# Optimization experiments

Hardware: AMD Instinct MI355X
Metric: run time of the kernel (lower is better)

The kernel has to match this reference:

```python
import jax, jax.numpy as jnp
import numpy as np

LN_EPS = 1e-5


def _layer_norm(x, g, b):
    mu = x.mean(-1, keepdims=True)
    var = ((x - mu) ** 2).mean(-1, keepdims=True)
    return (x - mu) / jnp.sqrt(var + LN_EPS) * g + b


def _process_memory(mem, mem_W, mem_b, ln_g, ln_b):
    # deep memory MLP: Linear -> LayerNorm -> SiLU per layer (dropout = identity in eval)
    h = mem
    for i in range(mem_W.shape[0]):
        h = jax.nn.silu(_layer_norm(h @ mem_W[i] + mem_b[i], ln_g[i], ln_b[i]))
    return h


def setup_inputs() -> dict:
    key = jax.random.key(0)
    B, S, D, M, L = 32, 2048, 1024, 1024, 2
    ks = jax.random.split(key, 12)
    s = 0.02
    inp = {
        'inputs': jax.random.normal(ks[0], (B, S, D), dtype=jnp.float32),
        'memory_state': jnp.zeros((B, M), dtype=jnp.float32),
        'momentum_state': jnp.zeros((B, M), dtype=jnp.float32),
        # projections (stored [in, out], equivalent to torch Linear weight.T)
        'Wk': jax.random.normal(ks[1], (D, M)) * s, 'bk': jnp.zeros((M,)),
        'Wv': jax.random.normal(ks[2], (D, M)) * s, 'bv': jnp.zeros((M,)),
        # deep memory layers, stacked over num_layers
        'mem_W': jax.random.normal(ks[3], (L, M, M)) * s,
        'mem_b': jnp.zeros((L, M)),
        'ln_g': jnp.ones((L, M)),
        'ln_b': jnp.zeros((L, M)),
        # gates: in = D + M
        'Wf': jax.random.normal(ks[4], (D + M, M)) * s, 'bf': jnp.zeros((M,)),
        'Wm': jax.random.normal(ks[5], (D + M, M)) * s, 'bm': jnp.zeros((M,)),
        'Wu': jax.random.normal(ks[6], (D + M, M)) * s, 'bu': jnp.zeros((M,)),
        'eta': jnp.ones((1,)) * 0.9,
        'theta': jnp.ones((1,)) * 0.1,
    }
    return inp


def reference(inputs, memory_state, momentum_state, Wk, bk, Wv, bv,
              mem_W, mem_b, ln_g, ln_b, Wf, bf, Wm, bm, Wu, bu, eta, theta):
    keys = inputs @ Wk + bk      # [B,S,M]
    values = inputs @ Wv + bv    # [B,S,M]

    def assoc_loss(mem):
        mo = _process_memory(mem, mem_W, mem_b, ln_g, ln_b)      # [B,M]
        pred = jnp.einsum('bsm,bm->bs', keys, mo)                # bmm(keys, mo^T)
        diff = pred[..., None] - values                          # expand to [B,S,M]
        return 0.5 * jnp.mean(diff ** 2)

    surprise_grad = jax.grad(assoc_loss)(memory_state)           # [B,M]

    pooled = inputs.mean(axis=1)                                 # [B,D]
    gate_in = jnp.concatenate([pooled, memory_state], axis=-1)   # [B,D+M]
    forget_g = jax.nn.sigmoid(gate_in @ Wf + bf)
    update_g = jax.nn.sigmoid(gate_in @ Wu + bu)
    # momentum_gate computed in source but unused in the update
    _ = jax.nn.sigmoid(gate_in @ Wm + bm)

    new_momentum = eta * momentum_state + theta * surprise_grad
    new_memory = (1.0 - forget_g) * memory_state + update_g * new_momentum

    processed = _process_memory(new_memory, mem_W, mem_b, ln_g, ln_b)
    return processed, jax.lax.stop_gradient(new_memory)
```

## Files before the change

### kernel.cpp

```cpp
#include <hip/hip_runtime.h>
#include <math.h>

#define Bc 32
#define Sc 2048
#define Dc 1024
#define Mc 1024
#define LNEPS 1e-5f
#define SCv (1.f/67108864.f)

__device__ __forceinline__ float4 f4add(float4 a, float4 b) {
    return make_float4(a.x + b.x, a.y + b.y, a.z + b.z, a.w + b.w);
}

__device__ __forceinline__ void dreduce(float& a, float& b, float* sm) {
#pragma unroll
    for (int o = 32; o; o >>= 1) { a += __shfl_xor(a, o); b += __shfl_xor(b, o); }
    int w = threadIdx.x >> 6;
    if ((threadIdx.x & 63) == 0) { sm[w] = a; sm[4 + w] = b; }
    __syncthreads();
    a = sm[0] + sm[1] + sm[2] + sm[3];
    b = sm[4] + sm[5] + sm[6] + sm[7];
    __syncthreads();
}

__device__ __forceinline__ void wreduce(float& a, float& b) {
#pragma unroll
    for (int o = 32; o; o >>= 1) { a += __shfl_xor(a, o); b += __shfl_xor(b, o); }
}

__device__ __forceinline__ void load_A128(float* Atile, const float* A, int b0, int k0) {
    for (int i = threadIdx.x; i < 1024; i += 256) {
        int r = i >> 7, c = i & 127;
        Atile[i] = A[(size_t)(b0 + r) * 1024 + k0 + c];
    }
}

__device__ __forceinline__ void nt_inner128v(const float* Atile, const float* W, int k0, int n0,
                                             float* P, int ks, int b0) {
    int lane = threadIdx.x & 63, bl = threadIdx.x >> 6;
    int n4 = lane & 15, kg = lane >> 4;
    const float* a0 = Atile + bl * 128;
    const float* a1 = Atile + (bl + 4) * 128;
    const float4* Wp = (const float4*)(W + (size_t)k0 * 1024 + n0);
    float4 acc0 = make_float4(0.f, 0.f, 0.f, 0.f);
    float4 acc1 = make_float4(0.f, 0.f, 0.f, 0.f);
#pragma unroll 8
    for (int i = 0; i < 32; ++i) {
        int k = i * 4 + kg;
        float4 w4 = Wp[(size_t)k * 256 + n4];
        float av0 = a0[k], av1 = a1[k];
        acc0.x = fmaf(av0, w4.x, acc0.x); acc0.y = fmaf(av0, w4.y, acc0.y);
        acc0.z = fmaf(av0, w4.z, acc0.z); acc0.w = fmaf(av0, w4.w, acc0.w);
        acc1.x = fmaf(av1, w4.x, acc1.x); acc1.y = fmaf(av1, w4.y, acc1.y);
        acc1.z = fmaf(av1, w4.z, acc1.z); acc1.w = fmaf(av1, w4.w, acc1.w);
    }
#pragma unroll
    for (int o = 16; o <= 32; o <<= 1) {
        acc0.x += __shfl_xor(acc0.x, o); acc0.y += __shfl_xor(acc0.y, o);
        acc0.z += __shfl_xor(acc0.z, o); acc0.w += __shfl_xor(acc0.w, o);
        acc1.x += __shfl_xor(acc1.x, o); acc1.y += __shfl_xor(acc1.y, o);
        acc1.z += __shfl_xor(acc1.z, o); acc1.w += __shfl_xor(acc1.w, o);
    }
    if (kg == 0) {
        size_t base = (size_t)ks * 32768 + n0 + 4 * n4;
        *(float4*)&P[base + (size_t)(b0 + bl) * 1024] = acc0;
        *(float4*)&P[base + (size_t)(b0 + bl + 4) * 1024] = acc1;
    }
}

__device__ __forceinline__ void t_inner(const float* Asl, const float* W,
                                        int dbase, int m0, float* outp) {
    int lane = threadIdx.x & 63, wv = threadIdx.x >> 6;
    int half = lane >> 5, m4 = lane & 31;
    float4 a4 = ((const float4*)Asl)[m4];
    int d0 = dbase + wv * 64 + half;
    float res = 0.f;
#pragma unroll 8
    for (int p = 0; p < 32; ++p) {
        int d = d0 + p * 2;
        float4 w4 = ((const float4*)(W + (size_t)d * 1024 + m0))[m4];
        float v = w4.x * a4.x + w4.y * a4.y + w4.z * a4.z + w4.w * a4.w;
#pragma unroll
        for (int o = 1; o < 32; o <<= 1) v += __shfl_xor(v, o);
        res = (m4 == p) ? v : res;
    }
    outp[wv * 64 + m4 * 2 + half] = res;
}

__global__ __launch_bounds__(256) void k_front(const float* __restrict__ Wv, const float* __restrict__ bv,
                        const float* __restrict__ mem, const float* __restrict__ W0,
                        float* __restrict__ wv_row, float* __restrict__ bvsum,
                        float* __restrict__ P1a) {
    __shared__ float shm[1032];
    int bid = blockIdx.x, tid = threadIdx.x;
    if (bid < 256) {
        float s1 = 0.f, s2 = 0.f, s3 = 0.f, s4 = 0.f;
        for (int m = tid; m < 1024; m += 256) {
            s1 += Wv[(size_t)bid * 1024 + m];
            s2 += Wv[(size_t)(bid + 256) * 1024 + m];
            s3 += Wv[(size_t)(bid + 512) * 1024 + m];
            s4 += Wv[(size_t)(bid + 768) * 1024 + m];
        }
        dreduce(s1, s2, shm + 1024);
        dreduce(s3, s4, shm + 1024);
        if (tid == 0) {
            wv_row[bid] = s1; wv_row[bid + 256] = s2;
            wv_row[bid + 512] = s3; wv_row[bid + 768] = s4;
        }
        if (bid == 0) {
            float v = 0.f, d2 = 0.f;
            for (int m = tid; m < 1024; m += 256) v += bv[m];
            dreduce(v, d2, shm + 1024);
            if (tid == 0) *bvsum = v;
        }
    } else {
        int t = bid - 256;
        int n0 = (t & 15) * 64, b0 = ((t >> 4) & 3) * 8, ks = t >> 6, k0 = ks * 128;
        load_A128(shm, mem, b0, k0);
        __syncthreads();
        nt_inner128v(shm, W0, k0, n0, P1a, ks, b0);
    }
}

__global__ __launch_bounds__(256) void k_gemm_ln(const float* __restrict__ P, const float* __restrict__ bias,
                          const float* __restrict__ g, const float* __restrict__ be,
                          const float* __restrict__ W1, float* __restrict__ Pout) {
    __shared__ float shm[1040];
    int bid = blockIdx.x, tid = threadIdx.x;
    int n0 = (bid & 15) * 64, b0 = ((bid >> 4) & 3) * 8, ks = bid >> 6, k0 = ks * 128;
    float* Atile = shm; float* stats = shm + 1024;
    int wv = tid >> 6, lane = tid & 63;
    const float4* b4 = (const float4*)bias;
    for (int rr = 0; rr < 2; ++rr) {
        int r = wv + rr * 4, b = b0 + r;
        float s = 0.f, sq = 0.f;
#pragma unroll
        for (int q = 0; q < 4; ++q) {
            int m4 = lane + 64 * q;
            float4 z4 = b4[m4];
#pragma unroll
            for (int k2 = 0; k2 < 8; ++k2) {
                float4 v = ((const float4*)(P + (size_t)k2 * 32768 + (size_t)b * 1024))[m4];
                z4 = f4add(z4, v);
            }
            int c0 = 4 * m4 - k0;
            if ((unsigned)c0 < 128u) *(float4*)(Atile + r * 128 + c0) = z4;
            s += z4.x + z4.y + z4.z + z4.w;
            sq += z4.x * z4.x + z4.y * z4.y + z4.z * z4.z + z4.w * z4.w;
        }
        wreduce(s, sq);
        if (lane == 0) {
            float mean = s * (1.f / 1024.f);
            stats[r] = mean;
            stats[8 + r] = rsqrtf(sq * (1.f / 1024.f) - mean * mean + LNEPS);
        }
    }
    __syncthreads();
    for (int i = tid; i < 1024; i += 256) {
        int r = i >> 7, c = i & 127, m = k0 + c;
        float xh = (Atile[i] - stats[r]) * stats[8 + r];
        float y = fmaf(xh, g[m], be[m]);
        float sg = 1.f / (1.f + __expf(-y));
        Atile[i] = y * sg;
    }
    __syncthreads();
    nt_inner128v(Atile, W1, k0, n0, Pout, ks, b0);
}

__global__ __launch_bounds__(256) void k_wpart(const float* __restrict__ P2a, const float* __restrict__ memb1,
                        const float* __restrict__ lng1, const float* __restrict__ lnb1,
                        const float* __restrict__ bk, const float* __restrict__ Wk,
                        float* __restrict__ wpart, float* __restrict__ cbpart) {
    __shared__ float shm[136];
    int bid = blockIdx.x, tid = threadIdx.x;
    int dc = bid & 3, b = (bid >> 2) & 31, mc = bid >> 7, m0 = mc * 128;
    float* red = shm + 128;
    float4 z4 = ((const float4*)memb1)[tid];
#pragma unroll
    for (int k2 = 0; k2 < 8; ++k2) {
        float4 v = ((const float4*)(P2a + (size_t)k2 * 32768 + (size_t)b * 1024))[tid];
        z4 = f4add(z4, v);
    }
    float s = z4.x + z4.y + z4.z + z4.w;
    float sq = z4.x * z4.x + z4.y * z4.y + z4.z * z4.z + z4.w * z4.w;
    int c0 = 4 * tid - m0;
    if ((unsigned)c0 < 128u) *(float4*)(shm + c0) = z4;
    dreduce(s, sq, red);
    float mean = s * (1.f / 1024.f);
    float rstd = rsqrtf(sq * (1.f / 1024.f) - mean * mean + LNEPS);
    if (tid < 128) {
        int m = m0 + tid;
        float xh = (shm[tid] - mean) * rstd;
        float y = fmaf(xh, lng1[m], lnb1[m]);
        float sg = 1.f / (1.f + __expf(-y));
        shm[tid] = y * sg;
    }
    __syncthreads();
    if (dc == 0) {
        float c = (tid < 128) ? bk[m0 + tid] * shm[tid] : 0.f;
        float d2 = 0.f;
        dreduce(c, d2, red);
        if (tid == 0) cbpart[mc * 32 + b] = c;
    }
    t_inner(shm, Wk, dc * 256, m0, wpart + (size_t)(mc * 32 + b) * 1024 + dc * 256);
}

__global__ __launch_bounds__(256) void k_bigpass(const float* __restrict__ X, const float* __restrict__ wpart,
                          const float* __restrict__ wv_row, const float* __restrict__ cbpart,
                          const float* __restrict__ bvsum,
                          float* __restrict__ t_part, float* __restrict__ p_part,
                          float* __restrict__ rs_part) {
    __shared__ float red[4][1024];
    __shared__ float rsum_s[4];
    int b = blockIdx.y, ch = blockIdx.x;
    int wv = threadIdx.x >> 6, lane = threadIdx.x & 63;
    float4 wreg[4], tacc[4], pacc[4];
    const float4* wp4 = (const float4*)wpart;
    const float4* wr4 = (const float4*)wv_row;
#pragma unroll
    for (int j = 0; j < 4; ++j) {
        int d4 = lane + 64 * j;
        float4 a = make_float4(0.f, 0.f, 0.f, 0.f);
#pragma unroll
        for (int mc = 0; mc < 8; ++mc) a = f4add(a, wp4[(size_t)(mc * 32 + b) * 256 + d4]);
        float4 wr = wr4[d4];
        wreg[j].x = 1024.f * a.x - wr.x;
        wreg[j].y = 1024.f * a.y - wr.y;
        wreg[j].z = 1024.f * a.z - wr.z;
        wreg[j].w = 1024.f * a.w - wr.w;
        tacc[j] = make_float4(0.f, 0.f, 0.f, 0.f);
        pacc[j] = make_float4(0.f, 0.f, 0.f, 0.f);
    }
    float cbs = 0.f;
#pragma unroll
    for (int mc = 0; mc < 8; ++mc) cbs += cbpart[mc * 32 + b];
    float cbv = 1024.f * cbs - *bvsum;
    float rloc = 0.f;
    int s0r = ch * 64 + wv * 16;
#pragma unroll 2
    for (int i = 0; i < 16; ++i) {
        const float4* xr = (const float4*)(X + ((size_t)b * Sc + s0r + i) * Dc);
        float4 x[4]; float pp = 0.f;
#pragma unroll
        for (int j = 0; j < 4; ++j) {
            x[j] = xr[lane + 64 * j];
            pp += x[j].x * wreg[j].x + x[j].y * wreg[j].y + x[j].z * wreg[j].z + x[j].w * wreg[j].w;
        }
#pragma unroll
        for (int o = 32; o; o >>= 1) pp += __shfl_xor(pp, o);
        float r = pp + cbv;
        rloc += r;
#pragma unroll
        for (int j = 0; j < 4; ++j) {
            tacc[j].x = fmaf(x[j].x, r, tacc[j].x);
            tacc[j].y = fmaf(x[j].y, r, tacc[j].y);
            tacc[j].z = fmaf(x[j].z, r, tacc[j].z);
            tacc[j].w = fmaf(x[j].w, r, tacc[j].w);
            pacc[j].x += x[j].x; pacc[j].y += x[j].y;
            pacc[j].z += x[j].z; pacc[j].w += x[j].w;
        }
    }
    float4* redv = (float4*)red[wv];
#pragma unroll
    for (int j = 0; j < 4; ++j) redv[lane + 64 * j] = tacc[j];
    if (lane == 0) rsum_s[wv] = rloc;
    __syncthreads();
    size_t pb = ((size_t)b * 32 + ch) * 1024;
    for (int j = 0; j < 4; ++j) {
        int d = threadIdx.x + 256 * j;
        t_part[pb + d] = red[0][d] + red[1][d] + red[2][d] + red[3][d];
    }
    if (threadIdx.x == 0) rs_part[b * 32 + ch] = rsum_s[0] + rsum_s[1] + rsum_s[2] + rsum_s[3];
    __syncthreads();
#pragma unroll
    for (int j = 0; j < 4; ++j) redv[lane + 64 * j] = pacc[j];
    __syncthreads();
    for (int j = 0; j < 4; ++j) {
        int d = threadIdx.x + 256 * j;
        p_part[pb + d] = red[0][d] + red[1][d] + red[2][d] + red[3][d];
    }
}

__global__ __launch_bounds__(256) void k_gates(const float* __restrict__ t_part, const float* __restrict__ p_part,
                        const float* __restrict__ mem,
                        const float* __restrict__ Wk, const float* __restrict__ Wf,
                        const float* __restrict__ Wu,
                        float* __restrict__ Pg, float* __restrict__ Pfp, float* __restrict__ Pup,
                        float* __restrict__ Pfm, float* __restrict__ Pum) {
    __shared__ float Atile[1024];
    int bid = blockIdx.x, tid = threadIdx.x;
    int z = bid >> 9, t = bid & 511;
    int n0 = (t & 15) * 64, b0 = ((t >> 4) & 3) * 8, ks = t >> 6, k0 = ks * 128;
    if (z >= 3) {
        load_A128(Atile, mem, b0, k0);
        __syncthreads();
        if (z == 3) nt_inner128v(Atile, Wf + (size_t)1024 * 1024, k0, n0, Pfm, ks, b0);
        else        nt_inner128v(Atile, Wu + (size_t)1024 * 1024, k0, n0, Pum, ks, b0);
        return;
    }
    const float* src = (z == 0) ? t_part : p_part;
    float scale = (z == 0) ? 1.f : (1.f / 2048.f);
    {
        int r = tid >> 5, c4 = tid & 31;
        int b = b0 + r;
        const float4* base = (const float4*)(src + (size_t)b * 32 * 1024 + k0) + c4;
        float4 acc = make_float4(0.f, 0.f, 0.f, 0.f);
#pragma unroll 8
        for (int ch = 0; ch < 32; ++ch) acc = f4add(acc, base[(size_t)ch * 256]);
        acc.x *= scale; acc.y *= scale; acc.z *= scale; acc.w *= scale;
        *(float4*)(Atile + r * 128 + 4 * c4) = acc;
    }
    __syncthreads();
    if (z == 0)      nt_inner128v(Atile, Wk, k0, n0, Pg, ks, b0);
    else if (z == 1) nt_inner128v(Atile, Wf, k0, n0, Pfp, ks, b0);
    else             nt_inner128v(Atile, Wu, k0, n0, Pup, ks, b0);
}

__global__ __launch_bounds__(256) void k_lnbwd_gemmT(const float* __restrict__ Pz, const float* __restrict__ bias,
                              const float* __restrict__ g, const float* __restrict__ be,
                              const float* __restrict__ Pgrad, int mode,
                              const float* __restrict__ bk, const float* __restrict__ rs_part,
                              const float* __restrict__ W, float* __restrict__ Pout) {
    __shared__ float shm[392];
    int bid = blockIdx.x, tid = threadIdx.x;
    int dc = bid & 3, b = (bid >> 2) & 31, mc = bid >> 7, m0 = mc * 128;
    float* red = shm + 384;
    float rsb = 0.f;
    if (mode) {
        float v = (tid < 32) ? rs_part[b * 32 + tid] : 0.f, d2 = 0.f;
        dreduce(v, d2, red);
        rsb = v;
    }
    float4 z4 = ((const float4*)bias)[tid];
#pragma unroll
    for (int k2 = 0; k2 < 8; ++k2) {
        float4 v = ((const float4*)(Pz + (size_t)k2 * 32768 + (size_t)b * 1024))[tid];
        z4 = f4add(z4, v);
    }
    float s = z4.x + z4.y + z4.z + z4.w;
    float sq = z4.x * z4.x + z4.y * z4.y + z4.z * z4.z + z4.w * z4.w;
    dreduce(s, sq, red);
    float mean = s * (1.f / 1024.f);
    float rstd = rsqrtf(sq * (1.f / 1024.f) - mean * mean + LNEPS);
    float4 g4 = make_float4(0.f, 0.f, 0.f, 0.f);
#pragma unroll
    for (int k2 = 0; k2 < 8; ++k2) {
        float4 v = ((const float4*)(Pgrad + (size_t)k2 * 32768 + (size_t)b * 1024))[tid];
        g4 = f4add(g4, v);
    }
    if (mode) {
        float4 bk4 = ((const float4*)bk)[tid];
        g4.x = SCv * (g4.x + bk4.x * rsb);
        g4.y = SCv * (g4.y + bk4.y * rsb);
        g4.z = SCv * (g4.z + bk4.z * rsb);
        g4.w = SCv * (g4.w + bk4.w * rsb);
    }
    float4 gg = ((const float4*)g)[tid], bb = ((const float4*)be)[tid];
    float sa = 0.f, sax = 0.f;
    float4 a4, xh4;
    {
        xh4.x = (z4.x - mean) * rstd;
        float y = fmaf(xh4.x, gg.x, bb.x);
        float sg2 = 1.f / (1.f + __expf(-y));
        a4.x = g4.x * (sg2 * (1.f + y * (1.f - sg2))) * gg.x;
        sa += a4.x; sax += a4.x * xh4.x;
        xh4.y = (z4.y - mean) * rstd;
        y = fmaf(xh4.y, gg.y, bb.y);
        sg2 = 1.f / (1.f + __expf(-y));
        a4.y = g4.y * (sg2 * (1.f + y * (1.f - sg2))) * gg.y;
        sa += a4.y; sax += a4.y * xh4.y;
        xh4.z = (z4.z - mean) * rstd;
        y = fmaf(xh4.z, gg.z, bb.z);
        sg2 = 1.f / (1.f + __expf(-y));
        a4.z = g4.z * (sg2 * (1.f + y * (1.f - sg2))) * gg.z;
        sa += a4.z; sax += a4.z * xh4.z;
        xh4.w = (z4.w - mean) * rstd;
        y = fmaf(xh4.w, gg.w, bb.w);
        sg2 = 1.f / (1.f + __expf(-y));
        a4.w = g4.w * (sg2 * (1.f + y * (1.f - sg2))) * gg.w;
        sa += a4.w; sax += a4.w * xh4.w;
    }
    int c0 = 4 * tid - m0;
    if ((unsigned)c0 < 128u) {
        *(float4*)(shm + c0) = a4;
        *(float4*)(shm + 128 + c0) = xh4;
    }
    dreduce(sa, sax, red);
    float ma = sa * (1.f / 1024.f), mx = sax * (1.f / 1024.f);
    if (tid < 128) shm[256 + tid] = rstd * (shm[tid] - ma - shm[128 + tid] * mx);
    __syncthreads();
    t_inner(shm + 256, W, dc * 256, m0, Pout + (size_t)(mc * 32 + b) * 1024 + dc * 256);
}

__global__ __launch_bounds__(256) void k_upd_g3(const float* __restrict__ Pfm, const float* __restrict__ Pfp,
                         const float* __restrict__ Pum, const float* __restrict__ Pup,
                         const float* __restrict__ surp,
                         const float* __restrict__ bf, const float* __restrict__ bu,
                         const float* __restrict__ mem, const float* __restrict__ mom,
                         const float* __restrict__ eta, const float* __restrict__ theta,
                         const float* __restrict__ W0, float* __restrict__ P3a,
                         float* __restrict__ out_nm) {
    __shared__ float Atile[1024];
    int bid = blockIdx.x, tid = threadIdx.x;
    int n0idx = bid & 15, n0 = n0idx * 64, b0 = ((bid >> 4) & 3) * 8, ks = bid >> 6, k0 = ks * 128;
    float etav = eta[0], thv = theta[0];
    int r = tid >> 5, c4 = tid & 31, b = b0 + r;
    int m4 = (k0 >> 2) + c4;
    float4 zf = ((const float4*)bf)[m4];
    float4 zu = ((const float4*)bu)[m4];
    float4 sv = make_float4(0.f, 0.f, 0.f, 0.f);
#pragma unroll
    for (int k2 = 0; k2 < 8; ++k2) {
        size_t ob4 = (size_t)k2 * 8192 + (size_t)b * 256 + m4;
        zf = f4add(zf, f4add(((const float4*)Pfm)[ob4], ((const float4*)Pfp)[ob4]));
        zu = f4add(zu, f4add(((const float4*)Pum)[ob4], ((const float4*)Pup)[ob4]));
        sv = f4add(sv, ((const float4*)surp)[ob4]);
    }
    float4 me = ((const float4*)mem)[(size_t)b * 256 + m4];
    float4 mo = ((const float4*)mom)[(size_t)b * 256 + m4];
    float4 nm;
    {
        float f = 1.f / (1.f + __expf(-zf.x)), u = 1.f / (1.f + __expf(-zu.x));
        nm.x = (1.f - f) * me.x + u * (etav * mo.x + thv * sv.x);
        f = 1.f / (1.f + __expf(-zf.y)); u = 1.f / (1.f + __expf(-zu.y));
        nm.y = (1.f - f) * me.y + u * (etav * mo.y + thv * sv.y);
        f = 1.f / (1.f + __expf(-zf.z)); u = 1.f / (1.f + __expf(-zu.z));
        nm.z = (1.f - f) * me.z + u * (etav * mo.z + thv * sv.z);
        f = 1.f / (1.f + __expf(-zf.w)); u = 1.f / (1.f + __expf(-zu.w));
        nm.w = (1.f - f) * me.w + u * (etav * mo.w + thv * sv.w);
    }
    *(float4*)(Atile + r * 128 + 4 * c4) = nm;
    if (n0idx == 0) ((float4*)out_nm)[(size_t)b * 256 + m4] = nm;
    __syncthreads();
    nt_inner128v(Atile, W0, k0, n0, P3a, ks, b0);
}

__global__ __launch_bounds__(256) void k_final(const float* __restrict__ P4a, const float* __restrict__ memb1,
                        const float* __restrict__ lng1, const float* __restrict__ lnb1,
                        float* __restrict__ out) {
    __shared__ float sm[8];
    int b = blockIdx.x, tid = threadIdx.x;
    float4 z4 = ((const float4*)memb1)[tid];
#pragma unroll
    for (int k2 = 0; k2 < 8; ++k2) {
        float4 v = ((const float4*)(P4a + (size_t)k2 * 32768 + (size_t)b * 1024))[tid];
        z4 = f4add(z4, v);
    }
    float s = z4.x + z4.y + z4.z + z4.w;
    float sq = z4.x * z4.x + z4.y * z4.y + z4.z * z4.z + z4.w * z4.w;
    dreduce(s, sq, sm);
    float mean = s * (1.f / 1024.f);
    float rstd = rsqrtf(sq * (1.f / 1024.f) - mean * mean + LNEPS);
    float4 gg = ((const float4*)lng1)[tid], bb = ((const float4*)lnb1)[tid];
    float4 o;
    {
        float xh = (z4.x - mean) * rstd, y = fmaf(xh, gg.x, bb.x);
        o.x = y / (1.f + __expf(-y));
        xh = (z4.y - mean) * rstd; y = fmaf(xh, gg.y, bb.y);
        o.y = y / (1.f + __expf(-y));
        xh = (z4.z - mean) * rstd; y = fmaf(xh, gg.z, bb.z);
        o.z = y / (1.f + __expf(-y));
        xh = (z4.w - mean) * rstd; y = fmaf(xh, gg.w, bb.w);
        o.w = y / (1.f + __expf(-y));
    }
    ((float4*)out)[(size_t)b * 256 + tid] = o;
}

extern "C" void kernel_launch(void* const* d_in, const int* in_sizes, int n_in,
                              void* d_out, int out_size, void* d_ws, size_t ws_size,
                              hipStream_t stream) {
    const float* X    = (const float*)d_in[0];
    const float* mem  = (const float*)d_in[1];
    const float* mom  = (const float*)d_in[2];
    const float* Wk   = (const float*)d_in[3];
    const float* bk   = (const float*)d_in[4];
    const float* Wv   = (const float*)d_in[5];
    const float* bv   = (const float*)d_in[6];
    const float* memW = (const float*)d_in[7];
    const float* memb = (const float*)d_in[8];
    const float* lng  = (const float*)d_in[9];
    const float* lnb  = (const float*)d_in[10];
    const float* Wf   = (const float*)d_in[11];
    const float* bf   = (const float*)d_in[12];
    const float* Wu   = (const float*)d_in[15];
    const float* bu   = (const float*)d_in[16];
    const float* eta  = (const float*)d_in[17];
    const float* theta= (const float*)d_in[18];
    float* out = (float*)d_out;

    const size_t BM = (size_t)Bc * Mc;
    float* ws = (float*)d_ws;
    float* P1a    = ws;
    float* P2a    = ws + 8 * BM;
    float* wpart  = ws + 16 * BM;
    float* Pg     = ws + 24 * BM;
    float* Pfp    = ws + 32 * BM;
    float* Pup    = ws + 40 * BM;
    float* Pfm    = ws + 48 * BM;
    float* Pum    = ws + 56 * BM;
    float* ghp    = ws + 64 * BM;
    float* surp   = ws + 72 * BM;
    float* P3a    = ws + 80 * BM;
    float* P4a    = ws + 88 * BM;
    float* t_part = ws + 96 * BM;
    float* p_part = ws + 128 * BM;
    float* wv_row = ws + 160 * BM;
    float* bvsum  = wv_row + 1024;
    float* cbpart = bvsum + 1;
    float* rs_part= cbpart + 256;

    const float* W0 = memW;
    const float* W1 = memW + (size_t)Mc * Mc;

    k_front<<<768, 256, 0, stream>>>(Wv, bv, mem, W0, wv_row, bvsum, P1a);
    k_gemm_ln<<<512, 256, 0, stream>>>(P1a, memb, lng, lnb, W1, P2a);
    k_wpart<<<1024, 256, 0, stream>>>(P2a, memb + 1024, lng + 1024, lnb + 1024, bk, Wk, wpart, cbpart);
    k_bigpass<<<dim3(32, 32), 256, 0, stream>>>(X, wpart, wv_row, cbpart, bvsum, t_part, p_part, rs_part);
    k_gates<<<2560, 256, 0, stream>>>(t_part, p_part, mem, Wk, Wf, Wu, Pg, Pfp, Pup, Pfm, Pum);
    k_lnbwd_gemmT<<<1024, 256, 0, stream>>>(P2a, memb + 1024, lng + 1024, lnb + 1024, Pg, 1, bk, rs_part, W1, ghp);
    k_lnbwd_gemmT<<<1024, 256, 0, stream>>>(P1a, memb, lng, lnb, ghp, 0, bk, rs_part, W0, surp);
    k_upd_g3<<<512, 256, 0, stream>>>(Pfm, Pfp, Pum, Pup, surp, bf, bu, mem, mom, eta, theta, W0, P3a, out + BM);
    k_gemm_ln<<<512, 256, 0, stream>>>(P3a, memb, lng, lnb, W1, P4a);
    k_final<<<32, 256, 0, stream>>>(P4a, memb + 1024, lng + 1024, lnb + 1024, out);
}
```

Baseline: 165.3 us.

## Remap block indices for XCD locality and hoist chunk reductions into a separate kernel

```diff
diff --git a/kernel.cpp b/kernel.cpp
--- a/kernel.cpp
+++ b/kernel.cpp
@@ -26,6 +26,21 @@
 __device__ __forceinline__ void wreduce(float& a, float& b) {
 #pragma unroll
     for (int o = 32; o; o >>= 1) { a += __shfl_xor(a, o); b += __shfl_xor(b, o); }
+}
+
+__device__ __forceinline__ void nt_map(int t, int& n0i, int& b0i, int& ks) {
+    int xcd = t & 7, rest = t >> 3;
+    b0i = rest & 3;
+    int q = rest >> 2;
+    int s = q * 8 + xcd;
+    ks = s >> 4; n0i = s & 15;
+}
+__device__ __forceinline__ void t_map(int t, int& dc, int& b, int& mc) {
+    int xcd = t & 7, rest = t >> 3;
+    b = rest & 31;
+    int q = rest >> 5;
+    int s = q * 8 + xcd;
+    dc = s >> 3; mc = s & 7;
 }
 
 __device__ __forceinline__ void load_A128(float* Atile, const float* A, int b0, int k0) {
@@ -114,8 +129,9 @@
             if (tid == 0) *bvsum = v;
         }
     } else {
-        int t = bid - 256;
-        int n0 = (t & 15) * 64, b0 = ((t >> 4) & 3) * 8, ks = t >> 6, k0 = ks * 128;
+        int n0i, b0i, ks;
+        nt_map(bid - 256, n0i, b0i, ks);
+        int n0 = n0i * 64, b0 = b0i * 8, k0 = ks * 128;
         load_A128(shm, mem, b0, k0);
         __syncthreads();
         nt_inner128v(shm, W0, k0, n0, P1a, ks, b0);
@@ -126,8 +142,10 @@
                           const float* __restrict__ g, const float* __restrict__ be,
                           const float* __restrict__ W1, float* __restrict__ Pout) {
     __shared__ float shm[1040];
-    int bid = blockIdx.x, tid = threadIdx.x;
-    int n0 = (bid & 15) * 64, b0 = ((bid >> 4) & 3) * 8, ks = bid >> 6, k0 = ks * 128;
+    int tid = threadIdx.x;
+    int n0i, b0i, ks;
+    nt_map(blockIdx.x, n0i, b0i, ks);
+    int n0 = n0i * 64, b0 = b0i * 8, k0 = ks * 128;
     float* Atile = shm; float* stats = shm + 1024;
     int wv = tid >> 6, lane = tid & 63;
     const float4* b4 = (const float4*)bias;
@@ -172,8 +190,10 @@
                         const float* __restrict__ bk, const float* __restrict__ Wk,
                         float* __restrict__ wpart, float* __restrict__ cbpart) {
     __shared__ float shm[136];
-    int bid = blockIdx.x, tid = threadIdx.x;
-    int dc = bid & 3, b = (bid >> 2) & 31, mc = bid >> 7, m0 = mc * 128;
+    int tid = threadIdx.x;
+    int dc, b, mc;
+    t_map(blockIdx.x, dc, b, mc);
+    int m0 = mc * 128;
     float* red = shm + 128;
     float4 z4 = ((const float4*)memb1)[tid];
 #pragma unroll
@@ -281,56 +301,67 @@
     }
 }
 
-__global__ __launch_bounds__(256) void k_gates(const float* __restrict__ t_part, const float* __restrict__ p_part,
+__global__ __launch_bounds__(256) void k_reduce(const float* __restrict__ t_part, const float* __restrict__ p_part,
+                         const float* __restrict__ rs_part,
+                         float* __restrict__ tbuf, float* __restrict__ pooled,
+                         float* __restrict__ rsv) {
+    int idx = blockIdx.x * 256 + threadIdx.x;
+    int b = idx >> 8, d4 = idx & 255;
+    const float4* tp = (const float4*)t_part + (size_t)b * 8192 + d4;
+    const float4* pp = (const float4*)p_part + (size_t)b * 8192 + d4;
+    float4 st = make_float4(0.f, 0.f, 0.f, 0.f);
+    float4 sp = make_float4(0.f, 0.f, 0.f, 0.f);
+#pragma unroll 8
+    for (int ch = 0; ch < 32; ++ch) {
+        st = f4add(st, tp[(size_t)ch * 256]);
+        sp = f4add(sp, pp[(size_t)ch * 256]);
+    }
+    ((float4*)tbuf)[idx] = st;
+    sp.x *= (1.f / 2048.f); sp.y *= (1.f / 2048.f);
+    sp.z *= (1.f / 2048.f); sp.w *= (1.f / 2048.f);
+    ((float4*)pooled)[idx] = sp;
+    if (blockIdx.x == 0 && threadIdx.x < 32) {
+        float s = 0.f;
+        for (int ch = 0; ch < 32; ++ch) s += rs_part[threadIdx.x * 32 + ch];
+        rsv[threadIdx.x] = s;
+    }
+}
+
+__global__ __launch_bounds__(256) void k_gates(const float* __restrict__ tbuf, const float* __restrict__ pooled,
                         const float* __restrict__ mem,
                         const float* __restrict__ Wk, const float* __restrict__ Wf,
                         const float* __restrict__ Wu,
                         float* __restrict__ Pg, float* __restrict__ Pfp, float* __restrict__ Pup,
                         float* __restrict__ Pfm, float* __restrict__ Pum) {
     __shared__ float Atile[1024];
-    int bid = blockIdx.x, tid = threadIdx.x;
-    int z = bid >> 9, t = bid & 511;
-    int n0 = (t & 15) * 64, b0 = ((t >> 4) & 3) * 8, ks = t >> 6, k0 = ks * 128;
-    if (z >= 3) {
-        load_A128(Atile, mem, b0, k0);
-        __syncthreads();
-        if (z == 3) nt_inner128v(Atile, Wf + (size_t)1024 * 1024, k0, n0, Pfm, ks, b0);
-        else        nt_inner128v(Atile, Wu + (size_t)1024 * 1024, k0, n0, Pum, ks, b0);
-        return;
-    }
-    const float* src = (z == 0) ? t_part : p_part;
-    float scale = (z == 0) ? 1.f : (1.f / 2048.f);
-    {
-        int r = tid >> 5, c4 = tid & 31;
-        int b = b0 + r;
-        const float4* base = (const float4*)(src + (size_t)b * 32 * 1024 + k0) + c4;
-        float4 acc = make_float4(0.f, 0.f, 0.f, 0.f);
-#pragma unroll 8
-        for (int ch = 0; ch < 32; ++ch) acc = f4add(acc, base[(size_t)ch * 256]);
-        acc.x *= scale; acc.y *= scale; acc.z *= scale; acc.w *= scale;
-        *(float4*)(Atile + r * 128 + 4 * c4) = acc;
-    }
-    __syncthreads();
-    if (z == 0)      nt_inner128v(Atile, Wk, k0, n0, Pg, ks, b0);
-    else if (z == 1) nt_inner128v(Atile, Wf, k0, n0, Pfp, ks, b0);
-    else             nt_inner128v(Atile, Wu, k0, n0, Pup, ks, b0);
+    int bid = blockIdx.x;
+    int z = bid >> 9;
+    int n0i, b0i, ks;
+    nt_map(bid & 511, n0i, b0i, ks);
+    int n0 = n0i * 64, b0 = b0i * 8, k0 = ks * 128;
+    const float* A; const float* W; float* P;
+    if (z == 0)      { A = tbuf;   W = Wk;                          P = Pg; }
+    else if (z == 1) { A = pooled; W = Wf;                          P = Pfp; }
+    else if (z == 2) { A = pooled; W = Wu;                          P = Pup; }
+    else if (z == 3) { A = mem;    W = Wf + (size_t)1024 * 1024;    P = Pfm; }
+    else             { A = mem;    W = Wu + (size_t)1024 * 1024;    P = Pum; }
+    load_A128(Atile, A, b0, k0);
+    __syncthreads();
+    nt_inner128v(Atile, W, k0, n0, P, ks, b0);
 }
 
 __global__ __launch_bounds__(256) void k_lnbwd_gemmT(const float* __restrict__ Pz, const float* __restrict__ bias,
                               const float* __restrict__ g, const float* __restrict__ be,
                               const float* __restrict__ Pgrad, int mode,
-                              const float* __restrict__ bk, const float* __restrict__ rs_part,
+                              const float* __restrict__ bk, const float* __restrict__ rsv,
                               const float* __restrict__ W, float* __restrict__ Pout) {
     __shared__ float shm[392];
-    int bid = blockIdx.x, tid = threadIdx.x;
-    int dc = bid & 3, b = (bid >> 2) & 31, mc = bid >> 7, m0 = mc * 128;
+    int tid = threadIdx.x;
+    int dc, b, mc;
+    t_map(blockIdx.x, dc, b, mc);
+    int m0 = mc * 128;
     float* red = shm + 384;
-    float rsb = 0.f;
-    if (mode) {
-        float v = (tid < 32) ? rs_part[b * 32 + tid] : 0.f, d2 = 0.f;
-        dreduce(v, d2, red);
-        rsb = v;
-    }
+    float rsb = mode ? rsv[b] : 0.f;
     float4 z4 = ((const float4*)bias)[tid];
 #pragma unroll
     for (int k2 = 0; k2 < 8; ++k2) {
@@ -401,8 +432,10 @@
                          const float* __restrict__ W0, float* __restrict__ P3a,
                          float* __restrict__ out_nm) {
     __shared__ float Atile[1024];
-    int bid = blockIdx.x, tid = threadIdx.x;
-    int n0idx = bid & 15, n0 = n0idx * 64, b0 = ((bid >> 4) & 3) * 8, ks = bid >> 6, k0 = ks * 128;
+    int tid = threadIdx.x;
+    int n0i, b0i, ks;
+    nt_map(blockIdx.x, n0i, b0i, ks);
+    int n0 = n0i * 64, b0 = b0i * 8, k0 = ks * 128;
     float etav = eta[0], thv = theta[0];
     int r = tid >> 5, c4 = tid & 31, b = b0 + r;
     int m4 = (k0 >> 2) + c4;
@@ -430,7 +463,7 @@
         nm.w = (1.f - f) * me.w + u * (etav * mo.w + thv * sv.w);
     }
     *(float4*)(Atile + r * 128 + 4 * c4) = nm;
-    if (n0idx == 0) ((float4*)out_nm)[(size_t)b * 256 + m4] = nm;
+    if (n0i == 0) ((float4*)out_nm)[(size_t)b * 256 + m4] = nm;
     __syncthreads();
     nt_inner128v(Atile, W0, k0, n0, P3a, ks, b0);
 }
@@ -504,10 +537,13 @@
     float* P4a    = ws + 88 * BM;
     float* t_part = ws + 96 * BM;
     float* p_part = ws + 128 * BM;
-    float* wv_row = ws + 160 * BM;
+    float* tbuf   = ws + 160 * BM;
+    float* pooled = ws + 161 * BM;
+    float* wv_row = ws + 162 * BM;
     float* bvsum  = wv_row + 1024;
     float* cbpart = bvsum + 1;
     float* rs_part= cbpart + 256;
+    float* rsv    = rs_part + 1024;
 
     const float* W0 = memW;
     const float* W1 = memW + (size_t)Mc * Mc;
@@ -516,9 +552,10 @@
     k_gemm_ln<<<512, 256, 0, stream>>>(P1a, memb, lng, lnb, W1, P2a);
     k_wpart<<<1024, 256, 0, stream>>>(P2a, memb + 1024, lng + 1024, lnb + 1024, bk, Wk, wpart, cbpart);
     k_bigpass<<<dim3(32, 32), 256, 0, stream>>>(X, wpart, wv_row, cbpart, bvsum, t_part, p_part, rs_part);
-    k_gates<<<2560, 256, 0, stream>>>(t_part, p_part, mem, Wk, Wf, Wu, Pg, Pfp, Pup, Pfm, Pum);
-    k_lnbwd_gemmT<<<1024, 256, 0, stream>>>(P2a, memb + 1024, lng + 1024, lnb + 1024, Pg, 1, bk, rs_part, W1, ghp);
-    k_lnbwd_gemmT<<<1024, 256, 0, stream>>>(P1a, memb, lng, lnb, ghp, 0, bk, rs_part, W0, surp);
+    k_reduce<<<32, 256, 0, stream>>>(t_part, p_part, rs_part, tbuf, pooled, rsv);
+    k_gates<<<2560, 256, 0, stream>>>(tbuf, pooled, mem, Wk, Wf, Wu, Pg, Pfp, Pup, Pfm, Pum);
+    k_lnbwd_gemmT<<<1024, 256, 0, stream>>>(P2a, memb + 1024, lng + 1024, lnb + 1024, Pg, 1, bk, rsv, W1, ghp);
+    k_lnbwd_gemmT<<<1024, 256, 0, stream>>>(P1a, memb, lng, lnb, ghp, 0, bk, rsv, W0, surp);
     k_upd_g3<<<512, 256, 0, stream>>>(Pfm, Pfp, Pum, Pup, surp, bf, bu, mem, mom, eta, theta, W0, P3a, out + BM);
     k_gemm_ln<<<512, 256, 0, stream>>>(P3a, memb, lng, lnb, W1, P4a);
     k_final<<<32, 256, 0, stream>>>(P4a, memb + 1024, lng + 1024, lnb + 1024, out);
```

Result: no change. 162.6 us (-1.6%).
